# Optimization experiments

Hardware: AMD Instinct MI355X
Metric: run time of the kernel (lower is better)

## Reference

```python
import jax, jax.numpy as jnp
import numpy as np

# Dimensions (all layers are mLSTM due to the constructor bug: `if w` tests the
# whole truthy `which` list, so signature=(2,1) still yields 3 mLSTM layers).
L, S, B, I = 3, 512, 4, 512      # layers, seq_len, batch, inp_dim
H, D = 8, 64                     # head_num, head_dim
HD = H * D                       # hidden dim = 512
P = 2 * I                        # up_l projection dim (m-branch p_factor = 2)
K = 4                            # causal conv kernel size
EPS = 1e-5
PNAMES = ['ln_g', 'ln_b', 'upl_w', 'upl_b', 'upr_w', 'upr_b', 'conv_w', 'conv_b',
          'wq_w', 'wq_b', 'wk_w', 'wk_b', 'wv_w', 'wv_b', 'wo_w', 'wo_b',
          'wi_w', 'wi_b', 'wf_w', 'wf_b', 'skip_w', 'gn_g', 'gn_b', 'down_w', 'down_b']


def setup_inputs() -> dict:
    key = jax.random.key(0)
    ks = iter(jax.random.split(key, 16))
    def w(shape, fan_in):
        return jax.random.normal(next(ks), shape, jnp.float32) / np.float32(np.sqrt(fan_in))
    return {
        'seq': jax.random.normal(next(ks), (S, B, I), jnp.float32),
        'ln_g': jnp.ones((L, I), jnp.float32), 'ln_b': jnp.zeros((L, I), jnp.float32),
        'upl_w': w((L, P, I), I), 'upl_b': jnp.zeros((L, P), jnp.float32),
        'upr_w': w((L, HD, I), I), 'upr_b': jnp.zeros((L, HD), jnp.float32),
        'conv_w': w((L, K), K), 'conv_b': jnp.zeros((L,), jnp.float32),
        'wq_w': w((L, HD, P), P), 'wq_b': jnp.zeros((L, HD), jnp.float32),
        'wk_w': w((L, HD, P), P), 'wk_b': jnp.zeros((L, HD), jnp.float32),
        'wv_w': w((L, HD, P), P), 'wv_b': jnp.zeros((L, HD), jnp.float32),
        'wo_w': w((L, HD, P), P), 'wo_b': jnp.zeros((L, HD), jnp.float32),
        'wi_w': w((L, H, P), P), 'wi_b': jnp.zeros((L, H), jnp.float32),
        'wf_w': w((L, H, P), P), 'wf_b': jnp.zeros((L, H), jnp.float32),
        'skip_w': w((L, HD, P), P),
        'gn_g': jnp.ones((L, HD), jnp.float32), 'gn_b': jnp.zeros((L, HD), jnp.float32),
        'down_w': w((L, I, HD), HD), 'down_b': jnp.zeros((L, I), jnp.float32),
    }


def _layernorm(x, g, b):
    mu = x.mean(-1, keepdims=True)
    v = ((x - mu) ** 2).mean(-1, keepdims=True)
    return (x - mu) / jnp.sqrt(v + EPS) * g + b


def _groupnorm(x, g, b):
    # GroupNorm(head_num, HD) on (B, HD): normalize each head's D channels
    xh = x.reshape(-1, H, D)
    mu = xh.mean(-1, keepdims=True)
    v = ((xh - mu) ** 2).mean(-1, keepdims=True)
    xn = (xh - mu) / jnp.sqrt(v + EPS)
    return (xn * g.reshape(H, D) + b.reshape(H, D)).reshape(-1, HD)


def _causal_conv(x, w, b):
    # 1-channel causal conv over the feature axis of the per-step vector (B, P)
    xp = jnp.pad(x, ((0, 0), (K - 1, 0)))
    y = b
    for k in range(K):  # K=4, static unroll
        y = y + w[k] * xp[:, k:k + x.shape[1]]
    return y


def _mlstm_step(p, x, state):
    c_, n_, m_ = state
    x_n = _layernorm(x, p['ln_g'], p['ln_b'])
    x_t = x_n @ p['upl_w'].T + p['upl_b']                 # (B, P)
    r_t = x_n @ p['upr_w'].T + p['upr_b']                 # (B, HD)
    x_c = jax.nn.silu(_causal_conv(x_t, p['conv_w'], p['conv_b']))
    q = (x_c @ p['wq_w'].T + p['wq_b']).reshape(-1, H, D)
    k = (x_c @ p['wk_w'].T + p['wk_b']).reshape(-1, H, D) / np.float32(np.sqrt(D))
    v = (x_t @ p['wv_w'].T + p['wv_b']).reshape(-1, H, D)
    i = x_c @ p['wi_w'].T + p['wi_b']                     # (B, H)
    f = x_c @ p['wf_w'].T + p['wf_b']                     # (B, H)
    o = jax.nn.sigmoid(x_t @ p['wo_w'].T + p['wo_b'])     # (B, HD)
    m = jnp.maximum(f + m_, i)                            # stabilizer
    ig = jnp.exp(i - m)
    fg = jnp.exp(f - m + m_)
    c = fg[..., None, None] * c_ + ig[..., None, None] * jnp.einsum('bhd,bhe->bhde', v, k)
    n = fg[..., None] * n_ + ig[..., None] * k
    num = jnp.einsum('bhde,bhe->bhd', c, q)
    den = jnp.maximum(jnp.abs(jnp.einsum('bhd,bhd->bh', n, q)), 1.0)[..., None]
    h = o * (num / den).reshape(-1, HD)
    out = _groupnorm(h, p['gn_g'], p['gn_b']) + x_c @ p['skip_w'].T
    out = out * jax.nn.silu(r_t)
    out = out @ p['down_w'].T + p['down_b']
    return out + x, (c, n, m)


def _forward(seq, params):
    b = seq.shape[1]
    def step(states, x_t):
        new_states = []
        inp = x_t
        for l in range(L):
            pl = {k: v[l] for k, v in params.items()}
            inp, st = _mlstm_step(pl, inp, states[l])
            new_states.append(st)
        return tuple(new_states), inp
    init = tuple((jnp.zeros((b, H, D, D), seq.dtype),
                  jnp.ones((b, H, D), seq.dtype),
                  jnp.zeros((b, H), seq.dtype)) for _ in range(L))
    _, out = jax.lax.scan(step, init, seq)
    return out  # (S, B, I)


def reference(seq, ln_g, ln_b, upl_w, upl_b, upr_w, upr_b, conv_w, conv_b,
              wq_w, wq_b, wk_w, wk_b, wv_w, wv_b, wo_w, wo_b,
              wi_w, wi_b, wf_w, wf_b, skip_w, gn_g, gn_b, down_w, down_b):
    params = dict(zip(PNAMES, [ln_g, ln_b, upl_w, upl_b, upr_w, upr_b, conv_w, conv_b,
                               wq_w, wq_b, wk_w, wk_b, wv_w, wv_b, wo_w, wo_b,
                               wi_w, wi_b, wf_w, wf_b, skip_w, gn_g, gn_b, down_w, down_b]))
    return _forward(seq, params)
```

## Files before the change

### kernel.cpp

```cpp
#include <hip/hip_runtime.h>
#include <hip/hip_bf16.h>
#include <cstdint>
#include <cstddef>

typedef short short8 __attribute__((ext_vector_type(8)));
typedef short short4v __attribute__((ext_vector_type(4)));
typedef float f32x4 __attribute__((ext_vector_type(4)));
typedef __hip_bfloat16 bf16;

#define NROW 2048
#define N1 1536
#define N2 1664
#define N3 1024
#define EPSV 1e-5f
#define NUMSZ ((size_t)32*512*64)

static __device__ __forceinline__ bf16 f2bf(float v){ return __float2bfloat16(v); }
static __device__ __forceinline__ float bfbits2f(short s){
  unsigned u = ((unsigned)(unsigned short)s) << 16;
  float f; __builtin_memcpy(&f, &u, 4); return f;
}
static __device__ __forceinline__ void split_bf(float v, bf16& h, bf16& l){
  h = __float2bfloat16(v);
  l = __float2bfloat16(v - __bfloat162float(h));
}

static __device__ __forceinline__ void gload16(const bf16* g, bf16* l){
  __builtin_amdgcn_global_load_lds(
      (const __attribute__((address_space(1))) void*)(g),
      (__attribute__((address_space(3))) void*)(l), 16, 0, 0);
}

#define MFMA __builtin_amdgcn_mfma_f32_16x16x32_bf16

__global__ __launch_bounds__(256) void pack_all(
    const float* __restrict__ upl, const float* __restrict__ upr,
    const float* __restrict__ wq,  const float* __restrict__ wk,
    const float* __restrict__ skp, const float* __restrict__ wi,
    const float* __restrict__ wf,  const float* __restrict__ wv,
    const float* __restrict__ wo,  const float* __restrict__ dw,
    const float* __restrict__ uplb, const float* __restrict__ uprb,
    const float* __restrict__ wqb,  const float* __restrict__ wkb,
    const float* __restrict__ wib,  const float* __restrict__ wfb,
    const float* __restrict__ wvb,  const float* __restrict__ wob,
    const float* __restrict__ dwb,
    bf16* __restrict__ W1h, bf16* __restrict__ W1l,
    bf16* __restrict__ W2h, bf16* __restrict__ W2l,
    bf16* __restrict__ W3h, bf16* __restrict__ W3l,
    bf16* __restrict__ W4h, bf16* __restrict__ W4l,
    float* __restrict__ b1, float* __restrict__ b2,
    float* __restrict__ b3, float* __restrict__ b4)
{
  int l = blockIdx.y;
  int bx = blockIdx.x;
  if (bx < 768){
    int r = bx*2 + (threadIdx.x >> 7);
    int c4 = threadIdx.x & 127;
    const float* src = (r < 1024) ? upl + ((size_t)l*1024 + r)*512
                                  : upr + ((size_t)l*512 + (r-1024))*512;
    size_t o = ((size_t)l*N1 + r)*512 + c4*4;
    f32x4 v = *(const f32x4*)(src + c4*4);
    short4v hh, ll;
    for (int e=0;e<4;e++){ bf16 h_,l_; split_bf(v[e],h_,l_);
      hh[e] = *(short*)&h_; ll[e] = *(short*)&l_; }
    *(short4v*)(W1h+o) = hh; *(short4v*)(W1l+o) = ll;
  } else if (bx < 2432){
    int r = bx - 768;
    int c4 = threadIdx.x;
    const float* src; float sc = 1.f;
    if (r < 512)        src = wq  + ((size_t)l*512 + r)*1024;
    else if (r < 1024){ src = wk  + ((size_t)l*512 + r-512)*1024; sc = 0.125f; }
    else if (r < 1536)  src = skp + ((size_t)l*512 + r-1024)*1024;
    else if (r < 1544)  src = wi  + ((size_t)l*8   + r-1536)*1024;
    else if (r < 1552)  src = wf  + ((size_t)l*8   + r-1544)*1024;
    else src = nullptr;
    size_t o = ((size_t)l*N2 + r)*1024 + c4*4;
    f32x4 v = src ? *(const f32x4*)(src + c4*4) : (f32x4){0.f,0.f,0.f,0.f};
    short4v hh, ll;
    for (int e=0;e<4;e++){ bf16 h_,l_; split_bf(v[e]*sc,h_,l_);
      hh[e] = *(short*)&h_; ll[e] = *(short*)&l_; }
    *(short4v*)(W2h+o) = hh; *(short4v*)(W2l+o) = ll;
  } else if (bx < 3456){
    int r = bx - 2432;
    int c4 = threadIdx.x;
    const float* src = (r < 512) ? wv + ((size_t)l*512 + r)*1024
                                 : wo + ((size_t)l*512 + (r-512))*1024;
    size_t o = ((size_t)l*N3 + r)*1024 + c4*4;
    f32x4 v = *(const f32x4*)(src + c4*4);
    short4v hh, ll;
    for (int e=0;e<4;e++){ bf16 h_,l_; split_bf(v[e],h_,l_);
      hh[e] = *(short*)&h_; ll[e] = *(short*)&l_; }
    *(short4v*)(W3h+o) = hh; *(short4v*)(W3l+o) = ll;
  } else if (bx < 3712){
    int r = (bx - 3456)*2 + (threadIdx.x >> 7);
    int c4 = threadIdx.x & 127;
    const float* src = dw + ((size_t)l*512 + r)*512;
    size_t o = ((size_t)l*512 + r)*512 + c4*4;
    f32x4 v = *(const f32x4*)(src + c4*4);
    short4v hh, ll;
    for (int e=0;e<4;e++){ bf16 h_,l_; split_bf(v[e],h_,l_);
      hh[e] = *(short*)&h_; ll[e] = *(short*)&l_; }
    *(short4v*)(W4h+o) = hh; *(short4v*)(W4l+o) = ll;
  } else {
    for (int j = threadIdx.x; j < N1; j += 256)
      b1[l*N1+j] = (j < 1024) ? uplb[l*1024+j] : uprb[l*512+j-1024];
    for (int j = threadIdx.x; j < N2; j += 256){
      float v = 0.f;
      if (j < 512)        v = wqb[l*512+j];
      else if (j < 1024)  v = wkb[l*512+j-512]*0.125f;
      else if (j < 1536)  v = 0.f;
      else if (j < 1544)  v = wib[l*8+j-1536];
      else if (j < 1552)  v = wfb[l*8+j-1544];
      b2[l*N2+j] = v;
    }
    for (int j = threadIdx.x; j < N3; j += 256)
      b3[l*N3+j] = (j < 512) ? wvb[l*512+j] : wob[l*512+j-512];
    for (int j = threadIdx.x; j < 512; j += 256)
      b4[l*512+j] = dwb[l*512+j];
  }
}

static __device__ __forceinline__ void gemm_core(
    bf16* __restrict__ sm,
    int bx, int by,
    const bf16* __restrict__ Ah, const bf16* __restrict__ Al,
    const bf16* __restrict__ Wh, const bf16* __restrict__ Wl,
    const float* __restrict__ bias, float* __restrict__ Cf,
    bf16* __restrict__ Cbh, bf16* __restrict__ Cbl,
    const float* __restrict__ resid, int N, int K, int lda)
{
  int tid = threadIdx.x;
  int lane = tid & 63, w = tid >> 6;
  int wr = w >> 2, wc = w & 3;
  int m0 = by*128, n0 = bx*128;
  int srow = tid >> 2, sslot = tid & 3;
  int gcol = ((sslot ^ (srow & 3)) * 8);
  const bf16* gAh = Ah + (size_t)(m0 + srow)*lda + gcol;
  const bf16* gAl = Al + (size_t)(m0 + srow)*lda + gcol;
  const bf16* gBh = Wh + (size_t)(n0 + srow)*K + gcol;
  const bf16* gBl = Wl + (size_t)(n0 + srow)*K + gcol;

  f32x4 acc[4][2];
  for (int i=0;i<4;i++) for (int j=0;j<2;j++) acc[i][j] = (f32x4){0.f,0.f,0.f,0.f};

  int r = lane & 15, g = lane >> 4;
  int xs = (g ^ (r & 3)) * 8;
  int aoff[4], boff[2];
  for (int mi=0;mi<4;mi++) aoff[mi] = (wr*64 + mi*16 + r)*32 + xs;
  for (int ni=0;ni<2;ni++) boff[ni] = (wc*32 + ni*16 + r)*32 + xs;

  int nt = K >> 5;
#define STAGE_T(base, kk) do{ bf16* _d = sm + (base) + tid*8; \
    gload16(gAh + (kk), _d); \
    gload16(gAl + (kk), _d + 4096); \
    gload16(gBh + (kk), _d + 8192); \
    gload16(gBl + (kk), _d + 12288); }while(0)

  STAGE_T(0, 0);
  asm volatile("s_waitcnt vmcnt(0)" ::: "memory");
  __builtin_amdgcn_s_barrier();

  for (int t = 0; t < nt; ++t){
    int cb = (t & 1) * 16384;
    if (t + 1 < nt) STAGE_T(16384 - cb, (t+1)*32);
    const bf16* sA = sm + cb;
    short8 ah[4], al[4], bh2[2], bl2[2];
    for (int mi=0;mi<4;mi++){
      ah[mi] = *(const short8*)(sA + aoff[mi]);
      al[mi] = *(const short8*)(sA + 4096 + aoff[mi]);
    }
    for (int ni=0;ni<2;ni++){
      bh2[ni] = *(const short8*)(sA + 8192 + boff[ni]);
      bl2[ni] = *(const short8*)(sA + 12288 + boff[ni]);
    }
    for (int mi=0;mi<4;mi++) for (int ni=0;ni<2;ni++)
      acc[mi][ni] = MFMA(ah[mi], bh2[ni], acc[mi][ni],0,0,0);
    for (int mi=0;mi<4;mi++) for (int ni=0;ni<2;ni++)
      acc[mi][ni] = MFMA(al[mi], bh2[ni], acc[mi][ni],0,0,0);
    for (int mi=0;mi<4;mi++) for (int ni=0;ni<2;ni++)
      acc[mi][ni] = MFMA(ah[mi], bl2[ni], acc[mi][ni],0,0,0);
    asm volatile("s_waitcnt vmcnt(0)" ::: "memory");
    __builtin_amdgcn_s_barrier();
  }
#undef STAGE_T

  for (int mi=0;mi<4;mi++) for (int ni=0;ni<2;ni++){
    int col = n0 + wc*32 + ni*16 + r;
    float bv = bias ? bias[col] : 0.f;
    for (int j=0;j<4;j++){
      int row = m0 + wr*64 + mi*16 + g*4 + j;
      float v = acc[mi][ni][j] + bv;
      size_t o = (size_t)row*N + col;
      if (resid) v += resid[o];
      if (Cf) Cf[o] = v;
      if (Cbh) split_bf(v, Cbh[o], Cbl[o]);
    }
  }
}

static __device__ __forceinline__ void gemm_core64(
    bf16* __restrict__ sm,
    int bx, int by,
    const bf16* __restrict__ Ah, const bf16* __restrict__ Al,
    const bf16* __restrict__ Wh, const bf16* __restrict__ Wl,
    const float* __restrict__ bias, float* __restrict__ Cf,
    bf16* __restrict__ Cbh, bf16* __restrict__ Cbl,
    const float* __restrict__ resid, int N, int K, int lda)
{
  int tid = threadIdx.x;
  int lane = tid & 63, w = tid >> 6;
  int m0 = by*64, n0 = bx*128;
  int srow = tid >> 2, sslot = tid & 3;
  int gcol = ((sslot ^ (srow & 3)) * 8);
  const bf16* gAh = Ah + (size_t)(m0 + srow)*lda + gcol;
  const bf16* gAl = Al + (size_t)(m0 + srow)*lda + gcol;
  const bf16* gBh = Wh + (size_t)(n0 + srow)*K + gcol;
  const bf16* gBl = Wl + (size_t)(n0 + srow)*K + gcol;
  size_t pstr = (size_t)64*K;

  f32x4 acc[4][2];
  for (int i=0;i<4;i++) for (int j=0;j<2;j++) acc[i][j] = (f32x4){0.f,0.f,0.f,0.f};

  int r = lane & 15, g = lane >> 4;
  int xs = (g ^ (r & 3)) * 8;
  int aoff[4], boff[2];
  for (int mi=0;mi<4;mi++) aoff[mi] = (mi*16 + r)*32 + xs;
  for (int ni=0;ni<2;ni++) boff[ni] = (w*32 + ni*16 + r)*32 + xs;

  int nt = K >> 5;
#define STAGE64(base, kk) do{ bf16* _d = sm + (base) + tid*8; \
    gload16(gAh + (kk), _d); \
    gload16(gAl + (kk), _d + 2048); \
    gload16(gBh + (kk), _d + 4096);  gload16(gBh + (kk) + pstr, _d + 6144); \
    gload16(gBl + (kk), _d + 8192);  gload16(gBl + (kk) + pstr, _d + 10240); }while(0)

  STAGE64(0, 0);
  asm volatile("s_waitcnt vmcnt(0)" ::: "memory");
  __builtin_amdgcn_s_barrier();

  for (int t = 0; t < nt; ++t){
    int cb = (t & 1) * 12288;
    if (t + 1 < nt) STAGE64(12288 - cb, (t+1)*32);
    const bf16* sA = sm + cb;
    short8 ah[4], al[4], bh2[2], bl2[2];
    for (int mi=0;mi<4;mi++){
      ah[mi] = *(const short8*)(sA + aoff[mi]);
      al[mi] = *(const short8*)(sA + 2048 + aoff[mi]);
    }
    for (int ni=0;ni<2;ni++){
      bh2[ni] = *(const short8*)(sA + 4096 + boff[ni]);
      bl2[ni] = *(const short8*)(sA + 8192 + boff[ni]);
    }
    for (int mi=0;mi<4;mi++) for (int ni=0;ni<2;ni++)
      acc[mi][ni] = MFMA(ah[mi], bh2[ni], acc[mi][ni],0,0,0);
    for (int mi=0;mi<4;mi++) for (int ni=0;ni<2;ni++)
      acc[mi][ni] = MFMA(al[mi], bh2[ni], acc[mi][ni],0,0,0);
    for (int mi=0;mi<4;mi++) for (int ni=0;ni<2;ni++)
      acc[mi][ni] = MFMA(ah[mi], bl2[ni], acc[mi][ni],0,0,0);
    asm volatile("s_waitcnt vmcnt(0)" ::: "memory");
    __builtin_amdgcn_s_barrier();
  }
#undef STAGE64

  for (int mi=0;mi<4;mi++) for (int ni=0;ni<2;ni++){
    int col = n0 + w*32 + ni*16 + r;
    float bv = bias ? bias[col] : 0.f;
    for (int j=0;j<4;j++){
      int row = m0 + mi*16 + g*4 + j;
      float v = acc[mi][ni][j] + bv;
      size_t o = (size_t)row*N + col;
      if (resid) v += resid[o];
      if (Cf) Cf[o] = v;
      if (Cbh) split_bf(v, Cbh[o], Cbl[o]);
    }
  }
}

__global__ __launch_bounds__(256) void gemm_s64(
    const bf16* __restrict__ Ah, const bf16* __restrict__ Al,
    const bf16* __restrict__ Wh, const bf16* __restrict__ Wl,
    const float* __restrict__ bias, float* __restrict__ Cf,
    bf16* __restrict__ Cbh, bf16* __restrict__ Cbl,
    const float* __restrict__ resid, int N, int K, int lda, int nbx)
{
  __shared__ bf16 sm[2*12288];
  int id = blockIdx.x;
  int cpx = gridDim.x >> 3;
  int swz = (id & 7)*cpx + (id >> 3);
  int by = swz / nbx, bx = swz - by*nbx;
  gemm_core64(sm, bx, by, Ah, Al, Wh, Wl, bias, Cf, Cbh, Cbl, resid, N, K, lda);
}

__global__ __launch_bounds__(512) void gemm23(
    const bf16* __restrict__ A2h, const bf16* __restrict__ A2l,
    const bf16* __restrict__ W2h, const bf16* __restrict__ W2l,
    const float* __restrict__ b2,
    bf16* __restrict__ c2h, bf16* __restrict__ c2l,
    const bf16* __restrict__ A3h, const bf16* __restrict__ A3l,
    const bf16* __restrict__ W3h, const bf16* __restrict__ W3l,
    const float* __restrict__ b3,
    bf16* __restrict__ c3h, bf16* __restrict__ c3l)
{
  __shared__ bf16 sm[2*4*4096];
  int id = blockIdx.x;
  int cpx = gridDim.x >> 3;
  int swz = (id & 7)*cpx + (id >> 3);
  int by = swz / 21, bx = swz - by*21;
  if (bx < 13)
    gemm_core(sm, bx, by, A2h, A2l, W2h, W2l, b2, nullptr, c2h, c2l,
              nullptr, N2, 1024, 1024);
  else
    gemm_core(sm, bx-13, by, A3h, A3l, W3h, W3l, b3, nullptr, c3h, c3l,
              nullptr, N3, 1024, N1);
}

__global__ __launch_bounds__(256) void ln_kernel(const float* __restrict__ x,
    const float* __restrict__ g, const float* __restrict__ bt,
    bf16* __restrict__ xnh, bf16* __restrict__ xnl)
{
  int row = blockIdx.x, t = threadIdx.x;
  float v0 = x[(size_t)row*512 + t], v1 = x[(size_t)row*512 + 256 + t];
  float s = v0 + v1, ss = v0*v0 + v1*v1;
  for (int m=1; m<64; m<<=1){ s += __shfl_xor(s,m); ss += __shfl_xor(ss,m); }
  __shared__ float sh[8];
  int w = t >> 6, lane = t & 63;
  if (lane == 0){ sh[w] = s; sh[4+w] = ss; }
  __syncthreads();
  s = sh[0]+sh[1]+sh[2]+sh[3]; ss = sh[4]+sh[5]+sh[6]+sh[7];
  float mu = s*(1.f/512.f), var = ss*(1.f/512.f) - mu*mu;
  float rs = rsqrtf(var + EPSV);
  float y0 = (v0-mu)*rs*g[t]     + bt[t];
  float y1 = (v1-mu)*rs*g[256+t] + bt[256+t];
  split_bf(y0, xnh[(size_t)row*512 + t],       xnl[(size_t)row*512 + t]);
  split_bf(y1, xnh[(size_t)row*512 + 256 + t], xnl[(size_t)row*512 + 256 + t]);
}

__global__ __launch_bounds__(256) void conv_kernel(
    const bf16* __restrict__ c1h, const bf16* __restrict__ c1l,
    const float* __restrict__ cw, const float* __restrict__ cb,
    bf16* __restrict__ xch, bf16* __restrict__ xcl)
{
  int row = blockIdx.x;
  size_t rb = (size_t)row*N1;
  float w0=cw[0], w1=cw[1], w2=cw[2], w3=cw[3], bb=cb[0];
  int j0 = threadIdx.x*4;
  float x[7];
  for (int k=0;k<3;k++){
    int j = j0-3+k;
    x[k] = (j>=0) ? (bfbits2f(*(const short*)(c1h+rb+j)) +
                     bfbits2f(*(const short*)(c1l+rb+j))) : 0.f;
  }
  short4v h4 = *(const short4v*)(c1h+rb+j0);
  short4v l4 = *(const short4v*)(c1l+rb+j0);
  for (int k=0;k<4;k++) x[3+k] = bfbits2f(h4[k]) + bfbits2f(l4[k]);
  for (int i=0;i<4;i++){
    float y = bb + w0*x[i] + w1*x[i+1] + w2*x[i+2] + w3*x[i+3];
    float sg = 1.f/(1.f + __expf(-y));
    size_t o = (size_t)row*1024 + j0 + i;
    split_bf(y*sg, xch[o], xcl[o]);
  }
}

__global__ __launch_bounds__(512) void vtrans_kernel(
    const bf16* __restrict__ c3h, const bf16* __restrict__ c3l,
    bf16* __restrict__ vTh, bf16* __restrict__ vTl)
{
  int bh = blockIdx.y, b = bh >> 3, h = bh & 7;
  int d0 = blockIdx.x*8;
  int s = threadIdx.x;
  size_t i = (size_t)(s*4+b)*N3 + h*64 + d0;
  short4v h0 = *(const short4v*)(c3h+i), h1 = *(const short4v*)(c3h+i+4);
  short4v l0 = *(const short4v*)(c3l+i), l1 = *(const short4v*)(c3l+i+4);
  for (int dd=0; dd<4; dd++){
    size_t o = ((size_t)bh*64 + d0+dd)*512 + s;
    *(short*)(vTh+o) = h0[dd];
    *(short*)(vTl+o) = l0[dd];
  }
  for (int dd=0; dd<4; dd++){
    size_t o = ((size_t)bh*64 + d0+4+dd)*512 + s;
    *(short*)(vTh+o) = h1[dd];
    *(short*)(vTl+o) = l1[dd];
  }
}

__global__ __launch_bounds__(256) void attn_kernel(
    const bf16* __restrict__ c2h, const bf16* __restrict__ c2l,
    const bf16* __restrict__ vTh, const bf16* __restrict__ vTl,
    float* __restrict__ rowt,
    float* __restrict__ num, float* __restrict__ denp)
{
  __shared__ bf16 Ph[32*64], Pl[32*64];
  __shared__ float cts[512];
  __shared__ float rtl[32];
  int lane = threadIdx.x & 63, w = threadIdx.x >> 6;
  int x = blockIdx.x;
  int tb = x >> 1, half = x & 1;
  int bh = blockIdx.y, b = bh >> 3, h = bh & 7;
  int t0 = tb*32;

  if (w == 0){
    double fv[8]; float iv[8];
    for (int j=0;j<8;j++){
      int t = lane*8 + j;
      size_t ro = (size_t)(t*4+b)*N2;
      fv[j] = (double)(bfbits2f(*(const short*)(c2h+ro+1544+h)) +
                       bfbits2f(*(const short*)(c2l+ro+1544+h)));
      iv[j] = bfbits2f(*(const short*)(c2h+ro+1536+h)) +
              bfbits2f(*(const short*)(c2l+ro+1536+h));
    }
    double ps[8]; double s = 0.0;
    for (int j=0;j<8;j++){ s += fv[j]; ps[j] = s; }
    double run = s;
    for (int o=1;o<64;o<<=1){
      double u = __shfl_up(run, o);
      if (lane >= o) run += u;
    }
    double excl = run - s;
    float ct[8];
    for (int j=0;j<8;j++){
      ct[j] = (float)((double)iv[j] - (excl + ps[j]));
      cts[lane*8+j] = ct[j];
    }
    float pm[8]; float mm = -3.0e38f;
    for (int j=0;j<8;j++){ mm = fmaxf(mm, ct[j]); pm[j] = mm; }
    float incl = mm;
    for (int o=1;o<64;o<<=1){
      float u = __shfl_up(incl, o);
      if (lane >= o) incl = fmaxf(incl, u);
    }
    float ex = __shfl_up(incl, 1);
    if (lane == 0) ex = -3.0e38f;
    for (int j=0;j<8;j++){
      int t = lane*8 + j;
      float rt_ = -fmaxf(0.f, fmaxf(ex, pm[j]));
      if (t >= t0 && t < t0+32){
        rtl[t - t0] = rt_;
        if (half == 0) rowt[bh*512 + t] = rt_;
      }
    }
  }
  __syncthreads();

  int r = lane & 15, g = lane >> 4;
  int rq = g*4;

  short8 qh[2][2], ql[2][2];
  for (int mi=0;mi<2;mi++) for (int k0=0;k0<2;k0++){
    size_t off = (size_t)((t0+mi*16+r)*4+b)*N2 + h*64 + k0*32 + g*8;
    qh[mi][k0] = *(const short8*)(c2h+off);
    ql[mi][k0] = *(const short8*)(c2l+off);
  }
  float rtv[2][4];
  for (int mi=0;mi<2;mi++) for (int j=0;j<4;j++) rtv[mi][j] = rtl[mi*16+rq+j];

  f32x4 accPV[2];
  for (int i=0;i<2;i++) accPV[i] = (f32x4){0.f,0.f,0.f,0.f};
  float rsum[2][4];
  for (int i=0;i<2;i++) for (int j=0;j<4;j++) rsum[i][j] = 0.f;

  int nsb = (tb >> 1) + 1;
  for (int sb=half; sb<nsb; sb+=2){
    int s0 = sb*64;
    f32x4 acc[2];
    for (int i=0;i<2;i++) acc[i] = (f32x4){0.f,0.f,0.f,0.f};
    short8 kh[2], kl[2];
    for (int k0=0;k0<2;k0++){
      size_t off = (size_t)((s0+w*16+r)*4+b)*N2 + 512 + h*64 + k0*32 + g*8;
      kh[k0] = *(const short8*)(c2h+off);
      kl[k0] = *(const short8*)(c2l+off);
    }
    for (int k0=0;k0<2;k0++){
      for (int mi=0;mi<2;mi++) acc[mi] = MFMA(qh[mi][k0], kh[k0], acc[mi],0,0,0);
      for (int mi=0;mi<2;mi++) acc[mi] = MFMA(ql[mi][k0], kh[k0], acc[mi],0,0,0);
      for (int mi=0;mi<2;mi++) acc[mi] = MFMA(qh[mi][k0], kl[k0], acc[mi],0,0,0);
    }
    int sl = w*16 + r;
    int s = s0 + sl;
    float ctv = cts[s];
    for (int mi=0;mi<2;mi++){
      for (int j=0;j<4;j++){
        int tloc = mi*16 + rq + j;
        int t = t0 + tloc;
        float wg = (s <= t) ? __expf(rtv[mi][j] + ctv) : 0.f;
        float gv = acc[mi][j] * wg;
        rsum[mi][j] += gv;
        int col = ((((sl>>3) ^ (tloc&7))<<3) | (sl&7));
        split_bf(gv, Ph[tloc*64+col], Pl[tloc*64+col]);
      }
    }
    __syncthreads();
    short8 vh[2], vl[2];
    for (int k0=0;k0<2;k0++){
      size_t off = ((size_t)bh*64 + w*16 + r)*512 + s0 + k0*32 + g*8;
      vh[k0] = *(const short8*)(vTh+off);
      vl[k0] = *(const short8*)(vTl+off);
    }
    for (int k0=0;k0<2;k0++){
      short8 ph[2], pl[2];
      for (int mi=0;mi<2;mi++){
        int tloc = mi*16 + r;
        int slot = (k0*4 + g) ^ (tloc&7);
        ph[mi] = *(const short8*)(&Ph[tloc*64 + slot*8]);
        pl[mi] = *(const short8*)(&Pl[tloc*64 + slot*8]);
      }
      for (int mi=0;mi<2;mi++) accPV[mi] = MFMA(ph[mi], vh[k0], accPV[mi],0,0,0);
      for (int mi=0;mi<2;mi++) accPV[mi] = MFMA(pl[mi], vh[k0], accPV[mi],0,0,0);
      for (int mi=0;mi<2;mi++) accPV[mi] = MFMA(ph[mi], vl[k0], accPV[mi],0,0,0);
    }
    __syncthreads();
  }

  float* nump = num + (size_t)half*NUMSZ;
  for (int mi=0;mi<2;mi++)
    for (int j=0;j<4;j++){
      int t = t0 + mi*16 + rq + j;
      nump[((size_t)bh*512 + t)*64 + w*16 + r] = accPV[mi][j];
    }
  for (int mi=0;mi<2;mi++)
    for (int j=0;j<4;j++){
      float v = rsum[mi][j];
      v += __shfl_xor(v,1); v += __shfl_xor(v,2);
      v += __shfl_xor(v,4); v += __shfl_xor(v,8);
      if (r == 0){
        int t = t0 + mi*16 + rq + j;
        denp[((size_t)bh*512 + t)*8 + half*4 + w] = v;
      }
    }
}

__global__ __launch_bounds__(512) void h_kernel(
    const float* __restrict__ num, const float* __restrict__ denp,
    const float* __restrict__ rowt,
    const bf16* __restrict__ c2h, const bf16* __restrict__ c2l,
    const bf16* __restrict__ c3h, const bf16* __restrict__ c3l,
    const bf16* __restrict__ c1h, const bf16* __restrict__ c1l,
    const float* __restrict__ gng, const float* __restrict__ gnb,
    bf16* __restrict__ oph, bf16* __restrict__ opl)
{
  int row = blockIdx.x, t = row >> 2, b = row & 3;
  int h = threadIdx.x >> 6, d = threadIdx.x & 63;
  int bh = b*8 + h;
  size_t bt = (size_t)bh*512 + t;
  size_t qo = (size_t)row*N2 + h*64 + d;
  float qs = bfbits2f(*(const short*)(c2h+qo)) + bfbits2f(*(const short*)(c2l+qo));
  for (int m=1; m<64; m<<=1) qs += __shfl_xor(qs, m);
  float dn = __expf(rowt[bt]) * qs;
  for (int p=0; p<8; p++) dn += denp[bt*8 + p];
  dn = fmaxf(fabsf(dn), 1.f);
  float nv = num[bt*64 + d] + num[NUMSZ + bt*64 + d];
  size_t io = (size_t)row*N3 + 512 + h*64 + d;
  float ov = bfbits2f(*(const short*)(c3h+io)) + bfbits2f(*(const short*)(c3l+io));
  float o = 1.f/(1.f + __expf(-ov));
  float hv = o * nv / dn;
  float s = hv, ss = hv*hv;
  for (int m=1; m<64; m<<=1){ s += __shfl_xor(s,m); ss += __shfl_xor(ss,m); }
  float mu = s*(1.f/64.f), var = ss*(1.f/64.f) - mu*mu;
  float gn = (hv - mu)*rsqrtf(var + EPSV)*gng[h*64+d] + gnb[h*64+d];
  size_t ks = (size_t)row*N2 + 1024 + h*64 + d;
  float sk = bfbits2f(*(const short*)(c2h+ks)) + bfbits2f(*(const short*)(c2l+ks));
  size_t kr = (size_t)row*N1 + 1024 + h*64 + d;
  float rv = bfbits2f(*(const short*)(c1h+kr)) + bfbits2f(*(const short*)(c1l+kr));
  float y = (gn + sk) * (rv/(1.f + __expf(-rv)));
  size_t oo = (size_t)row*512 + h*64 + d;
  split_bf(y, oph[oo], opl[oo]);
}

extern "C" void kernel_launch(void* const* d_in, const int* in_sizes, int n_in,
                              void* d_out, int out_size, void* d_ws, size_t ws_size,
                              hipStream_t stream)
{
  (void)in_sizes; (void)n_in; (void)out_size; (void)ws_size;
  const float* seq    = (const float*)d_in[0];
  const float* ln_g   = (const float*)d_in[1];
  const float* ln_b   = (const float*)d_in[2];
  const float* upl_w  = (const float*)d_in[3];
  const float* upl_b  = (const float*)d_in[4];
  const float* upr_w  = (const float*)d_in[5];
  const float* upr_b  = (const float*)d_in[6];
  const float* conv_w = (const float*)d_in[7];
  const float* conv_b = (const float*)d_in[8];
  const float* wq_w   = (const float*)d_in[9];
  const float* wq_b   = (const float*)d_in[10];
  const float* wk_w   = (const float*)d_in[11];
  const float* wk_b   = (const float*)d_in[12];
  const float* wv_w   = (const float*)d_in[13];
  const float* wv_b   = (const float*)d_in[14];
  const float* wo_w   = (const float*)d_in[15];
  const float* wo_b   = (const float*)d_in[16];
  const float* wi_w   = (const float*)d_in[17];
  const float* wi_b   = (const float*)d_in[18];
  const float* wf_w   = (const float*)d_in[19];
  const float* wf_b   = (const float*)d_in[20];
  const float* skip_w = (const float*)d_in[21];
  const float* gn_g   = (const float*)d_in[22];
  const float* gn_b   = (const float*)d_in[23];
  const float* down_w = (const float*)d_in[24];
  const float* down_b = (const float*)d_in[25];

  char* ws = (char*)d_ws;
  size_t off = 0;
  auto alloc = [&](size_t bytes)->char*{
    char* p = ws + off; off = (off + bytes + 255) & ~(size_t)255; return p;
  };
  bf16*  W1h = (bf16*)alloc((size_t)3*N1*512*2);
  bf16*  W1l = (bf16*)alloc((size_t)3*N1*512*2);
  bf16*  W2h = (bf16*)alloc((size_t)3*N2*1024*2);
  bf16*  W2l = (bf16*)alloc((size_t)3*N2*1024*2);
  bf16*  W3h = (bf16*)alloc((size_t)3*N3*1024*2);
  bf16*  W3l = (bf16*)alloc((size_t)3*N3*1024*2);
  bf16*  W4h = (bf16*)alloc((size_t)3*512*512*2);
  bf16*  W4l = (bf16*)alloc((size_t)3*512*512*2);
  float* b1  = (float*)alloc((size_t)3*N1*4);
  float* b2  = (float*)alloc((size_t)3*N2*4);
  float* b3  = (float*)alloc((size_t)3*N3*4);
  float* b4  = (float*)alloc((size_t)3*512*4);
  bf16*  xnh = (bf16*)alloc((size_t)NROW*512*2);
  bf16*  xnl = (bf16*)alloc((size_t)NROW*512*2);
  bf16*  c1h = (bf16*)alloc((size_t)NROW*N1*2);
  bf16*  c1l = (bf16*)alloc((size_t)NROW*N1*2);
  bf16*  xch = (bf16*)alloc((size_t)NROW*1024*2);
  bf16*  xcl = (bf16*)alloc((size_t)NROW*1024*2);
  bf16*  c2h = (bf16*)alloc((size_t)NROW*N2*2);
  bf16*  c2l = (bf16*)alloc((size_t)NROW*N2*2);
  bf16*  c3h = (bf16*)alloc((size_t)NROW*N3*2);
  bf16*  c3l = (bf16*)alloc((size_t)NROW*N3*2);
  bf16*  vTh = (bf16*)alloc((size_t)32*64*512*2);
  bf16*  vTl = (bf16*)alloc((size_t)32*64*512*2);
  float* rowt= (float*)alloc((size_t)32*512*4);
  float* denp= (float*)alloc((size_t)32*512*8*4);
  float* num = (float*)alloc((size_t)2*NUMSZ*4);
  bf16*  oph = (bf16*)alloc((size_t)NROW*512*2);
  bf16*  opl = (bf16*)alloc((size_t)NROW*512*2);
  float* xA  = (float*)alloc((size_t)NROW*512*4);
  float* xB  = (float*)alloc((size_t)NROW*512*4);

  pack_all<<<dim3(3713,3), 256, 0, stream>>>(
      upl_w, upr_w, wq_w, wk_w, skip_w, wi_w, wf_w, wv_w, wo_w, down_w,
      upl_b, upr_b, wq_b, wk_b, wi_b, wf_b, wv_b, wo_b, down_b,
      W1h, W1l, W2h, W2l, W3h, W3l, W4h, W4l, b1, b2, b3, b4);

  for (int l = 0; l < 3; l++){
    const float* x_in = (l == 0) ? seq : ((l == 1) ? xA : xB);
    float* x_out = (l == 0) ? xA : ((l == 1) ? xB : (float*)d_out);

    ln_kernel<<<NROW, 256, 0, stream>>>(x_in, ln_g + l*512, ln_b + l*512, xnh, xnl);
    gemm_s64<<<32*12, 256, 0, stream>>>(
        xnh, xnl, W1h + (size_t)l*N1*512, W1l + (size_t)l*N1*512,
        b1 + l*N1, nullptr, c1h, c1l, nullptr, N1, 512, 512, 12);
    conv_kernel<<<NROW, 256, 0, stream>>>(c1h, c1l, conv_w + l*4, conv_b + l,
                                          xch, xcl);
    gemm23<<<21*16, 512, 0, stream>>>(
        xch, xcl, W2h + (size_t)l*N2*1024, W2l + (size_t)l*N2*1024, b2 + l*N2,
        c2h, c2l,
        c1h, c1l, W3h + (size_t)l*N3*1024, W3l + (size_t)l*N3*1024, b3 + l*N3,
        c3h, c3l);
    vtrans_kernel<<<dim3(8,32), 512, 0, stream>>>(c3h, c3l, vTh, vTl);
    attn_kernel<<<dim3(32,32), 256, 0, stream>>>(c2h, c2l, vTh, vTl,
                                                 rowt, num, denp);
    h_kernel<<<NROW, 512, 0, stream>>>(num, denp, rowt, c2h, c2l, c3h, c3l,
                                       c1h, c1l, gn_g + l*512, gn_b + l*512,
                                       oph, opl);
    gemm_s64<<<32*4, 256, 0, stream>>>(
        oph, opl, W4h + (size_t)l*512*512, W4l + (size_t)l*512*512,
        b4 + l*512, x_out, nullptr, nullptr, x_in, 512, 512, 512, 4);
  }
}
```

Baseline: 431.0 us.

## Hoist gate cumsum into prep kernel and rebalance causal attention blocks

Moves the per-(batch,head) forget-gate cumulative sum and running-max computation out of every attention block into a separate prep kernel, which also does the V transpose through LDS so reads and writes are coalesced. The attention kernel drops the two-way split over key blocks and instead pairs short and long causal query tiles (tb and 15-tb) across adjacent blocks. This removes redundant scan work and the extra partial num/den buffers and their summation, at the cost of half as many attention blocks and a longer serial loop per block.

```diff
diff --git a/kernel.cpp b/kernel.cpp
--- a/kernel.cpp
+++ b/kernel.cpp
@@ -13,7 +13,6 @@
 #define N2 1664
 #define N3 1024
 #define EPSV 1e-5f
-#define NUMSZ ((size_t)32*512*64)
 
 static __device__ __forceinline__ bf16 f2bf(float v){ return __float2bfloat16(v); }
 static __device__ __forceinline__ float bfbits2f(short s){
@@ -361,84 +360,91 @@
   }
 }
 
-__global__ __launch_bounds__(512) void vtrans_kernel(
+__global__ __launch_bounds__(512) void prep_kernel(
     const bf16* __restrict__ c3h, const bf16* __restrict__ c3l,
-    bf16* __restrict__ vTh, bf16* __restrict__ vTl)
+    const bf16* __restrict__ c2h, const bf16* __restrict__ c2l,
+    bf16* __restrict__ vTh, bf16* __restrict__ vTl,
+    float* __restrict__ rowt, float* __restrict__ colt)
 {
   int bh = blockIdx.y, b = bh >> 3, h = bh & 7;
-  int d0 = blockIdx.x*8;
-  int s = threadIdx.x;
-  size_t i = (size_t)(s*4+b)*N3 + h*64 + d0;
-  short4v h0 = *(const short4v*)(c3h+i), h1 = *(const short4v*)(c3h+i+4);
-  short4v l0 = *(const short4v*)(c3l+i), l1 = *(const short4v*)(c3l+i+4);
-  for (int dd=0; dd<4; dd++){
-    size_t o = ((size_t)bh*64 + d0+dd)*512 + s;
-    *(short*)(vTh+o) = h0[dd];
-    *(short*)(vTl+o) = l0[dd];
-  }
-  for (int dd=0; dd<4; dd++){
-    size_t o = ((size_t)bh*64 + d0+4+dd)*512 + s;
-    *(short*)(vTh+o) = h1[dd];
-    *(short*)(vTl+o) = l1[dd];
+  if (blockIdx.x < 8){
+    __shared__ short th[64*66], tl[64*66];
+    int s0 = blockIdx.x*64;
+    int sl = threadIdx.x >> 3, d8 = (threadIdx.x & 7)*8;
+    size_t i = (size_t)((s0+sl)*4+b)*N3 + h*64 + d8;
+    short8 hv = *(const short8*)(c3h+i);
+    short8 lv = *(const short8*)(c3l+i);
+    for (int e=0;e<8;e++){
+      th[sl*66 + d8+e] = hv[e];
+      tl[sl*66 + d8+e] = lv[e];
+    }
+    __syncthreads();
+    int dl = threadIdx.x >> 3, s8 = (threadIdx.x & 7)*8;
+    short8 oh, ol;
+    for (int e=0;e<8;e++){
+      oh[e] = th[(s8+e)*66 + dl];
+      ol[e] = tl[(s8+e)*66 + dl];
+    }
+    size_t o = ((size_t)bh*64 + dl)*512 + s0 + s8;
+    *(short8*)(vTh+o) = oh;
+    *(short8*)(vTl+o) = ol;
+    return;
+  }
+  if (threadIdx.x >= 64) return;
+  int lane = threadIdx.x;
+  double fv[8]; float iv[8];
+  for (int j=0;j<8;j++){
+    int t = lane*8 + j;
+    size_t ro = (size_t)(t*4+b)*N2;
+    fv[j] = (double)(bfbits2f(*(const short*)(c2h+ro+1544+h)) +
+                     bfbits2f(*(const short*)(c2l+ro+1544+h)));
+    iv[j] = bfbits2f(*(const short*)(c2h+ro+1536+h)) +
+            bfbits2f(*(const short*)(c2l+ro+1536+h));
+  }
+  double ps[8]; double s = 0.0;
+  for (int j=0;j<8;j++){ s += fv[j]; ps[j] = s; }
+  double run = s;
+  for (int o=1;o<64;o<<=1){
+    double u = __shfl_up(run, o);
+    if (lane >= o) run += u;
+  }
+  double excl = run - s;
+  float ct[8];
+  for (int j=0;j<8;j++){
+    ct[j] = (float)((double)iv[j] - (excl + ps[j]));
+    colt[bh*512 + lane*8 + j] = ct[j];
+  }
+  float pm[8]; float mm = -3.0e38f;
+  for (int j=0;j<8;j++){ mm = fmaxf(mm, ct[j]); pm[j] = mm; }
+  float incl = mm;
+  for (int o=1;o<64;o<<=1){
+    float u = __shfl_up(incl, o);
+    if (lane >= o) incl = fmaxf(incl, u);
+  }
+  float ex = __shfl_up(incl, 1);
+  if (lane == 0) ex = -3.0e38f;
+  for (int j=0;j<8;j++){
+    float inc = fmaxf(ex, pm[j]);
+    rowt[bh*512 + lane*8 + j] = -fmaxf(0.f, inc);
   }
 }
 
 __global__ __launch_bounds__(256) void attn_kernel(
     const bf16* __restrict__ c2h, const bf16* __restrict__ c2l,
     const bf16* __restrict__ vTh, const bf16* __restrict__ vTl,
-    float* __restrict__ rowt,
+    const float* __restrict__ rowt, const float* __restrict__ colt,
     float* __restrict__ num, float* __restrict__ denp)
 {
   __shared__ bf16 Ph[32*64], Pl[32*64];
   __shared__ float cts[512];
-  __shared__ float rtl[32];
   int lane = threadIdx.x & 63, w = threadIdx.x >> 6;
   int x = blockIdx.x;
-  int tb = x >> 1, half = x & 1;
+  int tb = (x & 1) ? (15 - (x >> 1)) : (x >> 1);
   int bh = blockIdx.y, b = bh >> 3, h = bh & 7;
   int t0 = tb*32;
 
-  if (w == 0){
-    double fv[8]; float iv[8];
-    for (int j=0;j<8;j++){
-      int t = lane*8 + j;
-      size_t ro = (size_t)(t*4+b)*N2;
-      fv[j] = (double)(bfbits2f(*(const short*)(c2h+ro+1544+h)) +
-                       bfbits2f(*(const short*)(c2l+ro+1544+h)));
-      iv[j] = bfbits2f(*(const short*)(c2h+ro+1536+h)) +
-              bfbits2f(*(const short*)(c2l+ro+1536+h));
-    }
-    double ps[8]; double s = 0.0;
-    for (int j=0;j<8;j++){ s += fv[j]; ps[j] = s; }
-    double run = s;
-    for (int o=1;o<64;o<<=1){
-      double u = __shfl_up(run, o);
-      if (lane >= o) run += u;
-    }
-    double excl = run - s;
-    float ct[8];
-    for (int j=0;j<8;j++){
-      ct[j] = (float)((double)iv[j] - (excl + ps[j]));
-      cts[lane*8+j] = ct[j];
-    }
-    float pm[8]; float mm = -3.0e38f;
-    for (int j=0;j<8;j++){ mm = fmaxf(mm, ct[j]); pm[j] = mm; }
-    float incl = mm;
-    for (int o=1;o<64;o<<=1){
-      float u = __shfl_up(incl, o);
-      if (lane >= o) incl = fmaxf(incl, u);
-    }
-    float ex = __shfl_up(incl, 1);
-    if (lane == 0) ex = -3.0e38f;
-    for (int j=0;j<8;j++){
-      int t = lane*8 + j;
-      float rt_ = -fmaxf(0.f, fmaxf(ex, pm[j]));
-      if (t >= t0 && t < t0+32){
-        rtl[t - t0] = rt_;
-        if (half == 0) rowt[bh*512 + t] = rt_;
-      }
-    }
-  }
+  cts[threadIdx.x]       = colt[bh*512 + threadIdx.x];
+  cts[256 + threadIdx.x] = colt[bh*512 + 256 + threadIdx.x];
   __syncthreads();
 
   int r = lane & 15, g = lane >> 4;
@@ -451,7 +457,8 @@
     ql[mi][k0] = *(const short8*)(c2l+off);
   }
   float rtv[2][4];
-  for (int mi=0;mi<2;mi++) for (int j=0;j<4;j++) rtv[mi][j] = rtl[mi*16+rq+j];
+  for (int mi=0;mi<2;mi++) for (int j=0;j<4;j++)
+    rtv[mi][j] = rowt[bh*512 + t0 + mi*16 + rq + j];
 
   f32x4 accPV[2];
   for (int i=0;i<2;i++) accPV[i] = (f32x4){0.f,0.f,0.f,0.f};
@@ -459,7 +466,7 @@
   for (int i=0;i<2;i++) for (int j=0;j<4;j++) rsum[i][j] = 0.f;
 
   int nsb = (tb >> 1) + 1;
-  for (int sb=half; sb<nsb; sb+=2){
+  for (int sb=0; sb<nsb; ++sb){
     int s0 = sb*64;
     f32x4 acc[2];
     for (int i=0;i<2;i++) acc[i] = (f32x4){0.f,0.f,0.f,0.f};
@@ -510,11 +517,10 @@
     __syncthreads();
   }
 
-  float* nump = num + (size_t)half*NUMSZ;
   for (int mi=0;mi<2;mi++)
     for (int j=0;j<4;j++){
       int t = t0 + mi*16 + rq + j;
-      nump[((size_t)bh*512 + t)*64 + w*16 + r] = accPV[mi][j];
+      num[((size_t)bh*512 + t)*64 + w*16 + r] = accPV[mi][j];
     }
   for (int mi=0;mi<2;mi++)
     for (int j=0;j<4;j++){
@@ -523,7 +529,7 @@
       v += __shfl_xor(v,4); v += __shfl_xor(v,8);
       if (r == 0){
         int t = t0 + mi*16 + rq + j;
-        denp[((size_t)bh*512 + t)*8 + half*4 + w] = v;
+        denp[((size_t)bh*512 + t)*4 + w] = v;
       }
     }
 }
@@ -545,9 +551,9 @@
   float qs = bfbits2f(*(const short*)(c2h+qo)) + bfbits2f(*(const short*)(c2l+qo));
   for (int m=1; m<64; m<<=1) qs += __shfl_xor(qs, m);
   float dn = __expf(rowt[bt]) * qs;
-  for (int p=0; p<8; p++) dn += denp[bt*8 + p];
+  for (int p=0; p<4; p++) dn += denp[bt*4 + p];
   dn = fmaxf(fabsf(dn), 1.f);
-  float nv = num[bt*64 + d] + num[NUMSZ + bt*64 + d];
+  float nv = num[bt*64 + d];
   size_t io = (size_t)row*N3 + 512 + h*64 + d;
   float ov = bfbits2f(*(const short*)(c3h+io)) + bfbits2f(*(const short*)(c3l+io));
   float o = 1.f/(1.f + __expf(-ov));
@@ -627,8 +633,9 @@
   bf16*  vTh = (bf16*)alloc((size_t)32*64*512*2);
   bf16*  vTl = (bf16*)alloc((size_t)32*64*512*2);
   float* rowt= (float*)alloc((size_t)32*512*4);
-  float* denp= (float*)alloc((size_t)32*512*8*4);
-  float* num = (float*)alloc((size_t)2*NUMSZ*4);
+  float* colt= (float*)alloc((size_t)32*512*4);
+  float* denp= (float*)alloc((size_t)32*512*4*4);
+  float* num = (float*)alloc((size_t)32*512*64*4);
   bf16*  oph = (bf16*)alloc((size_t)NROW*512*2);
   bf16*  opl = (bf16*)alloc((size_t)NROW*512*2);
   float* xA  = (float*)alloc((size_t)NROW*512*4);
@@ -654,9 +661,10 @@
         c2h, c2l,
         c1h, c1l, W3h + (size_t)l*N3*1024, W3l + (size_t)l*N3*1024, b3 + l*N3,
         c3h, c3l);
-    vtrans_kernel<<<dim3(8,32), 512, 0, stream>>>(c3h, c3l, vTh, vTl);
-    attn_kernel<<<dim3(32,32), 256, 0, stream>>>(c2h, c2l, vTh, vTl,
-                                                 rowt, num, denp);
+    prep_kernel<<<dim3(9,32), 512, 0, stream>>>(c3h, c3l, c2h, c2l,
+                                                vTh, vTl, rowt, colt);
+    attn_kernel<<<dim3(16,32), 256, 0, stream>>>(c2h, c2l, vTh, vTl,
+                                                 rowt, colt, num, denp);
     h_kernel<<<NROW, 512, 0, stream>>>(num, denp, rowt, c2h, c2l, c3h, c3l,
                                        c1h, c1l, gn_g + l*512, gn_b + l*512,
                                        oph, opl);
```

After: 387.7 us. 1.11x faster.
